# Performance work log

Measured on AMD Instinct MI355X. Metric: run time of the kernel, lower is better.

## Reference

```python
import jax, jax.numpy as jnp
import numpy as np
import math

B, F, N, EMB, H, NC, L = 16, 60, 512, 128, 4, 27, 2
EPS = 1e-5


def _ln(x, g, b):
    m = x.mean(-1, keepdims=True)
    v = ((x - m) ** 2).mean(-1, keepdims=True)
    return (x - m) / jnp.sqrt(v + EPS) * g + b


def _bn(x, g, b):
    # BatchNorm1d in training mode: batch statistics over dim 0
    m = x.mean(0)
    v = ((x - m) ** 2).mean(0)
    return (x - m) / jnp.sqrt(v + EPS) * g + b


def _pos_encoding(S, D):
    pos = jnp.arange(S, dtype=jnp.float32)[:, None]
    div = jnp.exp(jnp.arange(0, D, 2, dtype=jnp.float32) * (-math.log(10000.0) / D))
    ang = pos * div  # [S, D/2]
    return jnp.stack([jnp.sin(ang), jnp.cos(ang)], axis=-1).reshape(S, D)


def setup_inputs():
    key = jax.random.key(0)
    ks = jax.random.split(key, 16)
    rn = lambda i, shape, s: (jax.random.normal(ks[i], shape) * s).astype(jnp.float32)
    z = lambda *shape: jnp.zeros(shape, jnp.float32)
    o = lambda *shape: jnp.ones(shape, jnp.float32)
    return {
        "x": jax.random.normal(ks[0], (B, F, N, 3), dtype=jnp.float32),
        "frame_length": jax.random.randint(ks[1], (B,), 1, F + 1, dtype=jnp.int32),
        # PointNet encoder (shared per-point MLP 3->64->128->EMB, max-pool)
        "enc_w1": rn(2, (3, 64), 0.3), "enc_b1": z(64),
        "enc_w2": rn(3, (64, 128), 0.1), "enc_b2": z(128),
        "enc_w3": rn(4, (128, EMB), 0.1), "enc_b3": z(EMB),
        "cls_token": rn(5, (1, 1, EMB), 0.02), "cls_pos": rn(6, (1, 1, EMB), 0.02),
        # 2-layer post-norm TransformerEncoder (d=128, h=4, ff=256)
        "in_w": rn(7, (L, 3 * EMB, EMB), 0.05), "in_b": z(L, 3 * EMB),
        "out_w": rn(8, (L, EMB, EMB), 0.05), "out_b": z(L, EMB),
        "ln1_g": o(L, EMB), "ln1_b": z(L, EMB),
        "ff1_w": rn(9, (L, 256, EMB), 0.05), "ff1_b": z(L, 256),
        "ff2_w": rn(10, (L, EMB, 256), 0.05), "ff2_b": z(L, EMB),
        "ln2_g": o(L, EMB), "ln2_b": z(L, EMB),
        # MLP head (weights stored [in, out])
        "fc1_w": rn(11, (2 * EMB, 128), 0.05), "fc1_b": z(128),
        "bn1_g": o(128), "bn1_b": z(128),
        "fc15_w": rn(12, (128, 64), 0.05), "fc15_b": z(64),
        "bn15_g": o(64), "bn15_b": z(64),
        "fc2_w": rn(13, (64, 32), 0.05), "fc2_b": z(32),
        "bn2_g": o(32), "bn2_b": z(32),
        "fc_w": rn(14, (32, NC), 0.05), "fc_b": z(NC),
    }


def _forward(x, frame_length, enc_w1, enc_b1, enc_w2, enc_b2, enc_w3, enc_b3,
             cls_token, cls_pos, in_w, in_b, out_w, out_b, ln1_g, ln1_b,
             ff1_w, ff1_b, ff2_w, ff2_b, ln2_g, ln2_b,
             fc1_w, fc1_b, bn1_g, bn1_b, fc15_w, fc15_b, bn15_g, bn15_b,
             fc2_w, fc2_b, bn2_g, bn2_b, fc_w, fc_b):
    dh = EMB // H
    # --- per-frame PointNet encoder, vectorized over (B, F) ---
    # (replaces the ragged Python loop; padded frames are masked to zero below,
    #  exactly matching y = zeros(...) filled only for valid frames)
    h = jax.nn.relu(jnp.einsum('bfnc,cd->bfnd', x, enc_w1) + enc_b1)
    h = jax.nn.relu(h @ enc_w2 + enc_b2)
    h = h @ enc_w3 + enc_b3
    y = h.max(axis=2)  # [B, F, EMB]
    valid = (jnp.arange(F)[None, :] < frame_length[:, None])  # [B, F]
    y = jnp.where(valid[..., None], y, 0.0)

    # --- cls token + sinusoidal positions ---
    pe = _pos_encoding(F, EMB)[None]  # [1, F, EMB]
    y = jnp.concatenate([jnp.broadcast_to(cls_token, (B, 1, EMB)), y], axis=1)
    pos = jnp.concatenate([cls_pos, pe], axis=1)
    y = y + pos  # [B, F+1, EMB]

    S = F + 1
    kpm = jnp.arange(S)[None, :] >= (frame_length + 1)[:, None]  # True = pad
    bias = jnp.where(kpm, -1e9, 0.0)[:, None, None, :]  # [B,1,1,S]

    for l in range(L):
        qkv = y @ in_w[l].T + in_b[l]  # [B,S,3*EMB]
        q, k, v = jnp.split(qkv, 3, axis=-1)
        q = q.reshape(B, S, H, dh).transpose(0, 2, 1, 3)
        k = k.reshape(B, S, H, dh).transpose(0, 2, 1, 3)
        v = v.reshape(B, S, H, dh).transpose(0, 2, 1, 3)
        scores = jnp.einsum('bhqd,bhkd->bhqk', q, k) / math.sqrt(dh) + bias
        attn = jax.nn.softmax(scores, axis=-1)
        o = jnp.einsum('bhqk,bhkd->bhqd', attn, v).transpose(0, 2, 1, 3).reshape(B, S, EMB)
        y = _ln(y + (o @ out_w[l].T + out_b[l]), ln1_g[l], ln1_b[l])
        ff = jax.nn.relu(y @ ff1_w[l].T + ff1_b[l]) @ ff2_w[l].T + ff2_b[l]
        y = _ln(y + ff, ln2_g[l], ln2_b[l])

    # --- ragged gather: cls output + last valid frame output ---
    z1 = y[:, 0, :]
    z2 = y[jnp.arange(B), frame_length]  # position frame_length[i] (cls offset)
    zc = jnp.concatenate([z1, z2], axis=1)  # [B, 2*EMB]

    lrelu = lambda t: jax.nn.leaky_relu(t, negative_slope=0.2)
    y1 = lrelu(_bn(zc @ fc1_w + fc1_b, bn1_g, bn1_b))
    y1 = lrelu(_bn(y1 @ fc15_w + fc15_b, bn15_g, bn15_b))
    y1 = lrelu(_bn(y1 @ fc2_w + fc2_b, bn2_g, bn2_b))
    return y1 @ fc_w + fc_b  # [B, NC]


def reference(x, frame_length, enc_w1, enc_b1, enc_w2, enc_b2, enc_w3, enc_b3,
              cls_token, cls_pos, in_w, in_b, out_w, out_b, ln1_g, ln1_b,
              ff1_w, ff1_b, ff2_w, ff2_b, ln2_g, ln2_b,
              fc1_w, fc1_b, bn1_g, bn1_b, fc15_w, fc15_b, bn15_g, bn15_b,
              fc2_w, fc2_b, bn2_g, bn2_b, fc_w, fc_b):
    return _forward(x, frame_length, enc_w1, enc_b1, enc_w2, enc_b2, enc_w3, enc_b3,
                    cls_token, cls_pos, in_w, in_b, out_w, out_b, ln1_g, ln1_b,
                    ff1_w, ff1_b, ff2_w, ff2_b, ln2_g, ln2_b,
                    fc1_w, fc1_b, bn1_g, bn1_b, fc15_w, fc15_b, bn15_g, bn15_b,
                    fc2_w, fc2_b, bn2_g, bn2_b, fc_w, fc_b)
```

## Files before the change

kernel.cpp:

```cpp
#include <hip/hip_runtime.h>
#include <math.h>

#define SS 61
#define EPSV 1e-5f

typedef __attribute__((ext_vector_type(8))) short bf16x8;
typedef __attribute__((ext_vector_type(4))) short s16x4;
typedef __attribute__((ext_vector_type(4))) float f32x4;

__device__ __forceinline__ short f2bf(float f){
  return __builtin_bit_cast(short, (__bf16)f);
}
__device__ __forceinline__ float bf2f(short s){
  unsigned u = ((unsigned)(unsigned short)s) << 16;
  return __builtin_bit_cast(float, u);
}
__device__ __forceinline__ bf16x8 pack8(f32x4 lo, f32x4 hi){
  bf16x8 r;
  r[0]=f2bf(lo[0]); r[1]=f2bf(lo[1]); r[2]=f2bf(lo[2]); r[3]=f2bf(lo[3]);
  r[4]=f2bf(hi[0]); r[5]=f2bf(hi[1]); r[6]=f2bf(hi[2]); r[7]=f2bf(hi[3]);
  return r;
}
__device__ __forceinline__ s16x4 pack4(f32x4 v){
  s16x4 r; r[0]=f2bf(v[0]); r[1]=f2bf(v[1]); r[2]=f2bf(v[2]); r[3]=f2bf(v[3]); return r;
}
#define YI(t,d) (((t)<<7) + ((d) ^ (((t)&7)<<2)))
#define OI(t,e) (((t)<<7) + ((e) ^ (((t)&7)<<2)))
#define FI(t,e) (((t)<<8) + ((e) ^ (((t)&7)<<2)))
#define VI(k,d) (((k)<<5) + ((d) ^ (((k)&7)<<2)))
#define H1A(pt,idx) ((pt)*128 + (((idx)*2) ^ (((pt)&7)<<4)))
#define H2A(pt,idx) ((pt)*256 + (((idx)*2) ^ (((pt)&15)<<4)))

__global__ __launch_bounds__(256) void prep_kernel(
    const float* __restrict__ ew1, const float* __restrict__ eb1,
    const float* __restrict__ ew2, const float* __restrict__ ew3,
    const float* __restrict__ in_w, const float* __restrict__ ow,
    const float* __restrict__ f1w, const float* __restrict__ f2w,
    const float* __restrict__ fc1w, const float* __restrict__ fc15w,
    const float* __restrict__ fc2w, const float* __restrict__ fcw,
    unsigned short* __restrict__ wbf)
{
  int s = blockIdx.x * 256 + threadIdx.x;
  int i = s & 7, lane = (s >> 3) & 63, frag = s >> 9;
  int c = lane & 15, g = lane >> 4;
  int sig = 16 * (i >> 2) + 4 * g + (i & 3);
  unsigned short outv;
  if (frag < 8) {
    int mt = frag & 3;
    float base = (sig < 3) ? ew1[sig * 64 + 16 * mt + c]
               : (sig == 3 ? eb1[16 * mt + c] : 0.f);
    short hv = f2bf(base);
    if (frag < 4) outv = (unsigned short)hv;
    else { float rv = base - bf2f(hv); outv = (unsigned short)f2bf(rv); }
  } else if (frag < 24) {
    int f = frag - 8; int mt = f >> 1, ks = f & 1;
    outv = (unsigned short)f2bf(ew2[(32 * ks + sig) * 128 + 16 * mt + c]);
  } else if (frag < 56) {
    int f = frag - 24; int mt = f >> 2, ks = f & 3;
    outv = (unsigned short)f2bf(ew3[(32 * ks + sig) * 128 + 16 * mt + c]);
  } else if (frag < 568) {
    int f = frag - 56; int l = f >> 8; f &= 255;
    float v;
    if (f < 96) { int tq = f >> 2, ks = f & 3;
      v = in_w[(size_t)l * 49152 + (size_t)(16 * tq + c) * 128 + 32 * ks + sig]; }
    else if (f < 128) { int f3 = f - 96; int t = f3 >> 2, ks = f3 & 3;
      v = ow[(size_t)l * 16384 + (size_t)(16 * t + c) * 128 + 32 * ks + sig]; }
    else if (f < 192) { int f3 = f - 128; int t = f3 >> 2, ks = f3 & 3;
      v = f1w[(size_t)l * 32768 + (size_t)(16 * t + c) * 128 + 32 * ks + sig]; }
    else { int f3 = f - 192; int t = f3 >> 3, ks = f3 & 7;
      v = f2w[(size_t)l * 32768 + (size_t)(16 * t + c) * 256 + 32 * ks + sig]; }
    outv = (unsigned short)f2bf(v);
  } else {
    int f = frag - 568;
    float v; int hl;
    if (f < 128) { hl = f >> 6; int f6 = f & 63; int mt = f6 >> 3, ks = f6 & 7;
      v = fc1w[(32 * ks + sig) * 128 + 16 * mt + c]; }
    else if (f < 160) { int f2_ = f - 128; hl = f2_ >> 4; int f4 = f2_ & 15; int mt = f4 >> 2, ks = f4 & 3;
      v = fc15w[(32 * ks + sig) * 64 + 16 * mt + c]; }
    else if (f < 168) { int f2_ = f - 160; hl = f2_ >> 2; int f4 = f2_ & 3; int mt = f4 >> 1, ks = f4 & 1;
      v = fc2w[(32 * ks + sig) * 32 + 16 * mt + c]; }
    else { int f2_ = f - 168; hl = f2_ >> 1; int mt = f2_ & 1; int m = 16 * mt + c;
      v = (m < 27) ? fcw[sig * 27 + m] : 0.f; }
    short hv = f2bf(v);
    outv = hl ? (unsigned short)f2bf(v - bf2f(hv)) : (unsigned short)hv;
  }
  wbf[s] = outv;
}

__global__ __launch_bounds__(256) void enc_kernel(
    const float* __restrict__ x,
    const float* __restrict__ eb2, const float* __restrict__ eb3,
    const unsigned short* __restrict__ wbf,
    float* __restrict__ ymax)
{
  __shared__ __align__(16) unsigned short h1p[64 * 64];
  __shared__ __align__(16) unsigned short h2p[64 * 128];
  __shared__ float pmerge[2][128];
  const int tid = threadIdx.x, lane = tid & 63, wv = tid >> 6;
  const int c = lane & 15, g = lane >> 4;
  const int mh = wv & 1, gh = wv >> 1;
  const int frame = blockIdx.x;
  const bf16x8* wf = (const bf16x8*)wbf;

  bf16x8 A1h[4], A1l[4];
#pragma unroll
  for (int mt = 0; mt < 4; mt++) { A1h[mt] = wf[mt * 64 + lane]; A1l[mt] = wf[(4 + mt) * 64 + lane]; }
  bf16x8 A2f[4][2];
#pragma unroll
  for (int j = 0; j < 4; j++)
#pragma unroll
    for (int ks = 0; ks < 2; ks++) A2f[j][ks] = wf[(8 + (4 * mh + j) * 2 + ks) * 64 + lane];
  bf16x8 A3f[4][4];
#pragma unroll
  for (int j = 0; j < 4; j++)
#pragma unroll
    for (int ks = 0; ks < 4; ks++) A3f[j][ks] = wf[(24 + (4 * mh + j) * 4 + ks) * 64 + lane];
  f32x4 b2v[4];
#pragma unroll
  for (int j = 0; j < 4; j++) b2v[j] = *(const f32x4*)(eb2 + 16 * (4 * mh + j) + 4 * g);

  f32x4 pool[4];
#pragma unroll
  for (int j = 0; j < 4; j++) pool[j] = {-1e30f, -1e30f, -1e30f, -1e30f};

  const float* xf = x + (size_t)frame * 1536;
  float nx0, nx1, nx2;
  { const float* xp = xf + (16 * wv + c) * 3; nx0 = xp[0]; nx1 = xp[1]; nx2 = xp[2]; }

  const int ptw = 16 * wv + c;

  for (int t = 0; t < 8; t++) {
    const float x0 = nx0, x1 = nx1, x2 = nx2;
    if (t < 7) {
      const float* xp = xf + ((t + 1) * 64 + 16 * wv + c) * 3;
      nx0 = xp[0]; nx1 = xp[1]; nx2 = xp[2];
    }
    bf16x8 bxh = {0,0,0,0,0,0,0,0}, bxl = {0,0,0,0,0,0,0,0};
    if (g == 0) {
      short h0 = f2bf(x0), h1_ = f2bf(x1), h2_ = f2bf(x2);
      bxh[0] = h0; bxh[1] = h1_; bxh[2] = h2_; bxh[3] = (short)0x3F80;
      bxl[0] = f2bf(x0 - bf2f(h0)); bxl[1] = f2bf(x1 - bf2f(h1_)); bxl[2] = f2bf(x2 - bf2f(h2_));
    }
#pragma unroll
    for (int mt = 0; mt < 4; mt++) {
      f32x4 a = {0.f, 0.f, 0.f, 0.f};
      a = __builtin_amdgcn_mfma_f32_16x16x32_bf16(A1h[mt], bxh, a, 0, 0, 0);
      a = __builtin_amdgcn_mfma_f32_16x16x32_bf16(A1h[mt], bxl, a, 0, 0, 0);
      a = __builtin_amdgcn_mfma_f32_16x16x32_bf16(A1l[mt], bxh, a, 0, 0, 0);
      f32x4 rl;
#pragma unroll
      for (int r = 0; r < 4; r++) rl[r] = fmaxf(a[r], 0.f);
      *(s16x4*)((char*)h1p + H1A(ptw, (mt >> 1) * 32 + g * 8 + (mt & 1) * 4)) = pack4(rl);
    }
    __syncthreads();
    bf16x8 B2[2][2];
#pragma unroll
    for (int gi = 0; gi < 2; gi++)
#pragma unroll
      for (int ks = 0; ks < 2; ks++) {
        const int pt = 16 * (2 * gh + gi) + c;
        B2[gi][ks] = *(const bf16x8*)((const char*)h1p + H1A(pt, ks * 32 + g * 8));
      }
#pragma unroll
    for (int j = 0; j < 4; j++)
#pragma unroll
      for (int gi = 0; gi < 2; gi++) {
        f32x4 a = b2v[j];
        a = __builtin_amdgcn_mfma_f32_16x16x32_bf16(A2f[j][0], B2[gi][0], a, 0, 0, 0);
        a = __builtin_amdgcn_mfma_f32_16x16x32_bf16(A2f[j][1], B2[gi][1], a, 0, 0, 0);
        f32x4 rl;
#pragma unroll
        for (int r = 0; r < 4; r++) rl[r] = fmaxf(a[r], 0.f);
        const int mt = 4 * mh + j;
        const int pt = 16 * (2 * gh + gi) + c;
        *(s16x4*)((char*)h2p + H2A(pt, (mt >> 1) * 32 + g * 8 + (mt & 1) * 4)) = pack4(rl);
      }
    __syncthreads();
    bf16x8 B3[2][4];
#pragma unroll
    for (int gi = 0; gi < 2; gi++)
#pragma unroll
      for (int ks = 0; ks < 4; ks++) {
        const int pt = 16 * (2 * gh + gi) + c;
        B3[gi][ks] = *(const bf16x8*)((const char*)h2p + H2A(pt, ks * 32 + g * 8));
      }
#pragma unroll
    for (int j = 0; j < 4; j++)
#pragma unroll
      for (int gi = 0; gi < 2; gi++) {
        f32x4 a = {0.f, 0.f, 0.f, 0.f};
        a = __builtin_amdgcn_mfma_f32_16x16x32_bf16(A3f[j][0], B3[gi][0], a, 0, 0, 0);
        a = __builtin_amdgcn_mfma_f32_16x16x32_bf16(A3f[j][1], B3[gi][1], a, 0, 0, 0);
        a = __builtin_amdgcn_mfma_f32_16x16x32_bf16(A3f[j][2], B3[gi][2], a, 0, 0, 0);
        a = __builtin_amdgcn_mfma_f32_16x16x32_bf16(A3f[j][3], B3[gi][3], a, 0, 0, 0);
#pragma unroll
        for (int r = 0; r < 4; r++) pool[j][r] = fmaxf(pool[j][r], a[r]);
      }
  }

#pragma unroll
  for (int j = 0; j < 4; j++)
#pragma unroll
    for (int r = 0; r < 4; r++) {
      float v = pool[j][r];
      v = fmaxf(v, __shfl_xor(v, 1, 64));
      v = fmaxf(v, __shfl_xor(v, 2, 64));
      v = fmaxf(v, __shfl_xor(v, 4, 64));
      v = fmaxf(v, __shfl_xor(v, 8, 64));
      pool[j][r] = v;
    }
  if (c == 0) {
#pragma unroll
    for (int j = 0; j < 4; j++)
      *(f32x4*)&pmerge[gh][64 * mh + 16 * j + 4 * g] = pool[j];
  }
  __syncthreads();
  if (tid < 128)
    ymax[(size_t)frame * 128 + tid] = fmaxf(pmerge[0][tid], pmerge[1][tid]) + eb3[tid];
}

__global__ __launch_bounds__(512, 1) void xformer_kernel(
    const float* __restrict__ ymax, const int* __restrict__ fl,
    const float* __restrict__ ctok, const float* __restrict__ cpos,
    const unsigned short* __restrict__ wbf,
    const float* __restrict__ in_b, const float* __restrict__ ob,
    const float* __restrict__ l1g, const float* __restrict__ l1b,
    const float* __restrict__ f1b, const float* __restrict__ f2b,
    const float* __restrict__ l2g, const float* __restrict__ l2b,
    float* __restrict__ zbuf)
{
  __shared__ __align__(16) float ylds[64 * 128];
  __shared__ __align__(16) unsigned short ubuf[64 * 256];
  __shared__ __align__(16) unsigned short kq4[2][8][4][64][4];
  const int b = blockIdx.x, tid = threadIdx.x;
  const int w8 = tid >> 6, lane = tid & 63, c = lane & 15, g = lane >> 4;
  const int h = w8 >> 1, sub = w8 & 1;
  const int flb = fl[b];
  const float scl = 0.17677669529663687f;

  for (int it = 0; it < 16; it++) {
    int idx = it * 512 + tid;
    int t = idx >> 7, d = idx & 127;
    float v;
    if (t == 0) v = ctok[d] + cpos[d];
    else if (t <= 60) {
      int f = t - 1;
      float ym = (f < flb) ? ymax[(size_t)(b * 60 + f) * 128 + d] : 0.f;
      float dv = __expf((float)(d & ~1) * (-0.07195578416f));
      float ang = (float)f * dv;
      v = ym + ((d & 1) ? __cosf(ang) : __sinf(ang));
    } else v = 0.f;
    ylds[YI(t, d)] = v;
  }
  __syncthreads();

  for (int l = 0; l < 2; l++) {
    const unsigned short* WL = wbf + 28672 + (size_t)l * 131072;
    const bf16x8* wq  = (const bf16x8*)WL;
    const bf16x8* wo  = (const bf16x8*)(WL + 49152);
    const bf16x8* w1p = (const bf16x8*)(WL + 65536);
    const bf16x8* w2p = (const bf16x8*)(WL + 98304);
    unsigned short* vb = ubuf + 8192 + h * 2048;

    {
      bf16x8 yB[4][4];
#pragma unroll
      for (int nt = 0; nt < 4; nt++)
#pragma unroll
        for (int ks = 0; ks < 4; ks++) {
          f32x4 lo = *(const f32x4*)&ylds[YI(16 * nt + c, 32 * ks + 4 * g)];
          f32x4 hi = *(const f32x4*)&ylds[YI(16 * nt + c, 32 * ks + 16 + 4 * g)];
          yB[nt][ks] = pack8(lo, hi);
        }
#pragma unroll
      for (int p = 0; p < 3; p++) {
        const int tq = p * 8 + w8;
        bf16x8 Af[4];
#pragma unroll
        for (int ks = 0; ks < 4; ks++) Af[ks] = wq[(tq * 4 + ks) * 64 + lane];
        f32x4 bias = *(const f32x4*)(in_b + l * 384 + p * 128 + 16 * w8 + 4 * g);
        f32x4 acc[4];
#pragma unroll
        for (int nt = 0; nt < 4; nt++) acc[nt] = bias;
#pragma unroll
        for (int ks = 0; ks < 4; ks++)
#pragma unroll
          for (int nt = 0; nt < 4; nt++)
            acc[nt] = __builtin_amdgcn_mfma_f32_16x16x32_bf16(Af[ks], yB[nt][ks], acc[nt], 0, 0, 0);
        if (p == 2) {
#pragma unroll
          for (int nt = 0; nt < 4; nt++)
            *(s16x4*)&vb[VI(16 * nt + c, 16 * sub + 4 * g)] = pack4(acc[nt]);
        } else {
#pragma unroll
          for (int nt = 0; nt < 4; nt++) {
            f32x4 sv = acc[nt];
            if (p == 0) sv = sv * scl;
            *(s16x4*)&kq4[p][w8][nt][lane][0] = pack4(sv);
          }
        }
      }
    }
    __syncthreads();

    {
      bf16x8 Ak[4], Bq2[2];
#pragma unroll
      for (int kt = 0; kt < 4; kt++) {
        s16x4 lo = *(const s16x4*)&kq4[1][2 * h][kt][lane][0];
        s16x4 hi = *(const s16x4*)&kq4[1][2 * h + 1][kt][lane][0];
        Ak[kt] = __builtin_shufflevector(lo, hi, 0, 1, 2, 3, 4, 5, 6, 7);
      }
#pragma unroll
      for (int j = 0; j < 2; j++) {
        s16x4 lo = *(const s16x4*)&kq4[0][2 * h][2 * sub + j][lane][0];
        s16x4 hi = *(const s16x4*)&kq4[0][2 * h + 1][2 * sub + j][lane][0];
        Bq2[j] = __builtin_shufflevector(lo, hi, 0, 1, 2, 3, 4, 5, 6, 7);
      }
      f32x4 St[4][2];
#pragma unroll
      for (int kt = 0; kt < 4; kt++)
#pragma unroll
        for (int j = 0; j < 2; j++) {
          f32x4 z = {0.f, 0.f, 0.f, 0.f};
          St[kt][j] = __builtin_amdgcn_mfma_f32_16x16x32_bf16(Ak[kt], Bq2[j], z, 0, 0, 0);
        }
#pragma unroll
      for (int j = 0; j < 2; j++) {
        float m = -1e30f;
#pragma unroll
        for (int kt = 0; kt < 4; kt++)
#pragma unroll
          for (int r = 0; r < 4; r++) {
            const int kp = 16 * kt + 4 * g + r;
            float s = St[kt][j][r];
            s = (kp > flb) ? -1e30f : s;
            St[kt][j][r] = s;
            m = fmaxf(m, s);
          }
        m = fmaxf(m, __shfl_xor(m, 16, 64));
        m = fmaxf(m, __shfl_xor(m, 32, 64));
        float sum = 0.f;
#pragma unroll
        for (int kt = 0; kt < 4; kt++)
#pragma unroll
          for (int r = 0; r < 4; r++) {
            float p = __expf(St[kt][j][r] - m);
            St[kt][j][r] = p;
            sum += p;
          }
        sum += __shfl_xor(sum, 16, 64);
        sum += __shfl_xor(sum, 32, 64);
        const float inv = 1.f / sum;
#pragma unroll
        for (int kt = 0; kt < 4; kt++)
#pragma unroll
          for (int r = 0; r < 4; r++) St[kt][j][r] *= inv;
      }
      bf16x8 Bp[2][2];
#pragma unroll
      for (int j = 0; j < 2; j++)
#pragma unroll
        for (int ks = 0; ks < 2; ks++) {
          bf16x8 r;
#pragma unroll
          for (int i = 0; i < 8; i++) r[i] = f2bf(St[2 * ks + (i >> 2)][j][i & 3]);
          Bp[j][ks] = r;
        }
      bf16x8 Av[2][2];
#pragma unroll
      for (int dt = 0; dt < 2; dt++)
#pragma unroll
        for (int ks = 0; ks < 2; ks++) {
          bf16x8 r;
#pragma unroll
          for (int i = 0; i < 8; i++) {
            const int kp = 32 * ks + 16 * (i >> 2) + 4 * g + (i & 3);
            r[i] = (short)vb[VI(kp, 16 * dt + c)];
          }
          Av[dt][ks] = r;
        }
#pragma unroll
      for (int dt = 0; dt < 2; dt++)
#pragma unroll
        for (int j = 0; j < 2; j++) {
          f32x4 z = {0.f, 0.f, 0.f, 0.f};
          z = __builtin_amdgcn_mfma_f32_16x16x32_bf16(Av[dt][0], Bp[j][0], z, 0, 0, 0);
          z = __builtin_amdgcn_mfma_f32_16x16x32_bf16(Av[dt][1], Bp[j][1], z, 0, 0, 0);
          *(s16x4*)&ubuf[OI(16 * (2 * sub + j) + c, 32 * h + 16 * dt + 4 * g)] = pack4(z);
        }
    }
    __syncthreads();

    {
      bf16x8 Bo[4][4];
#pragma unroll
      for (int nt = 0; nt < 4; nt++)
#pragma unroll
        for (int ks = 0; ks < 4; ks++) {
          s16x4 lo = *(const s16x4*)&ubuf[OI(16 * nt + c, 32 * ks + 4 * g)];
          s16x4 hi = *(const s16x4*)&ubuf[OI(16 * nt + c, 32 * ks + 16 + 4 * g)];
          Bo[nt][ks] = __builtin_shufflevector(lo, hi, 0, 1, 2, 3, 4, 5, 6, 7);
        }
      const int j0 = 16 * w8;
      bf16x8 Af[4];
#pragma unroll
      for (int ks = 0; ks < 4; ks++) Af[ks] = wo[(w8 * 4 + ks) * 64 + lane];
      f32x4 bias = *(const f32x4*)(ob + l * 128 + j0 + 4 * g);
      f32x4 acc[4];
#pragma unroll
      for (int nt = 0; nt < 4; nt++) acc[nt] = bias;
#pragma unroll
      for (int ks = 0; ks < 4; ks++)
#pragma unroll
        for (int nt = 0; nt < 4; nt++)
          acc[nt] = __builtin_amdgcn_mfma_f32_16x16x32_bf16(Af[ks], Bo[nt][ks], acc[nt], 0, 0, 0);
#pragma unroll
      for (int nt = 0; nt < 4; nt++) {
        float* yp = &ylds[YI(16 * nt + c, j0 + 4 * g)];
        *(f32x4*)yp = *(const f32x4*)yp + acc[nt];
      }
    }
    __syncthreads();
    {
      const int t = 8 * w8 + (lane >> 3);
      const int s = lane & 7;
      f32x4 vv[4];
      float s1 = 0.f, s2 = 0.f;
#pragma unroll
      for (int k = 0; k < 4; k++) {
        vv[k] = *(const f32x4*)&ylds[YI(t, s * 16 + 4 * k)];
#pragma unroll
        for (int r = 0; r < 4; r++) { s1 += vv[k][r]; s2 = fmaf(vv[k][r], vv[k][r], s2); }
      }
      s1 += __shfl_xor(s1, 1, 64); s1 += __shfl_xor(s1, 2, 64); s1 += __shfl_xor(s1, 4, 64);
      s2 += __shfl_xor(s2, 1, 64); s2 += __shfl_xor(s2, 2, 64); s2 += __shfl_xor(s2, 4, 64);
      const float mean = s1 * 0.0078125f;
      const float var  = s2 * 0.0078125f - mean * mean;
      const float inv  = rsqrtf(var + EPSV);
#pragma unroll
      for (int k = 0; k < 4; k++) {
        f32x4 gg = *(const f32x4*)(l1g + l * 128 + s * 16 + 4 * k);
        f32x4 bb = *(const f32x4*)(l1b + l * 128 + s * 16 + 4 * k);
        f32x4 o;
#pragma unroll
        for (int r = 0; r < 4; r++) o[r] = (vv[k][r] - mean) * inv * gg[r] + bb[r];
        *(f32x4*)&ylds[YI(t, s * 16 + 4 * k)] = o;
      }
    }
    __syncthreads();

    {
      bf16x8 yB[4][4];
#pragma unroll
      for (int nt = 0; nt < 4; nt++)
#pragma unroll
        for (int ks = 0; ks < 4; ks++) {
          f32x4 lo = *(const f32x4*)&ylds[YI(16 * nt + c, 32 * ks + 4 * g)];
          f32x4 hi = *(const f32x4*)&ylds[YI(16 * nt + c, 32 * ks + 16 + 4 * g)];
          yB[nt][ks] = pack8(lo, hi);
        }
#pragma unroll
      for (int half = 0; half < 2; half++) {
        const int t16 = 8 * half + w8;
        bf16x8 Af[4];
#pragma unroll
        for (int ks = 0; ks < 4; ks++) Af[ks] = w1p[(t16 * 4 + ks) * 64 + lane];
        f32x4 bias = *(const f32x4*)(f1b + l * 256 + 16 * t16 + 4 * g);
        f32x4 acc[4];
#pragma unroll
        for (int nt = 0; nt < 4; nt++) acc[nt] = bias;
#pragma unroll
        for (int ks = 0; ks < 4; ks++)
#pragma unroll
          for (int nt = 0; nt < 4; nt++)
            acc[nt] = __builtin_amdgcn_mfma_f32_16x16x32_bf16(Af[ks], yB[nt][ks], acc[nt], 0, 0, 0);
#pragma unroll
        for (int nt = 0; nt < 4; nt++) {
          f32x4 rl;
#pragma unroll
          for (int r = 0; r < 4; r++) rl[r] = fmaxf(acc[nt][r], 0.f);
          *(s16x4*)&ubuf[FI(16 * nt + c, 16 * t16 + 4 * g)] = pack4(rl);
        }
      }
    }
    __syncthreads();
    {
      f32x4 acc[4];
      f32x4 bias = *(const f32x4*)(f2b + l * 128 + 16 * w8 + 4 * g);
#pragma unroll
      for (int nt = 0; nt < 4; nt++) acc[nt] = bias;
#pragma unroll
      for (int ks = 0; ks < 8; ks++) {
        bf16x8 Af = w2p[(w8 * 8 + ks) * 64 + lane];
        bf16x8 Bf[4];
#pragma unroll
        for (int nt = 0; nt < 4; nt++) {
          s16x4 lo = *(const s16x4*)&ubuf[FI(16 * nt + c, 32 * ks + 4 * g)];
          s16x4 hi = *(const s16x4*)&ubuf[FI(16 * nt + c, 32 * ks + 16 + 4 * g)];
          Bf[nt] = __builtin_shufflevector(lo, hi, 0, 1, 2, 3, 4, 5, 6, 7);
        }
#pragma unroll
        for (int nt = 0; nt < 4; nt++)
          acc[nt] = __builtin_amdgcn_mfma_f32_16x16x32_bf16(Af, Bf[nt], acc[nt], 0, 0, 0);
      }
#pragma unroll
      for (int nt = 0; nt < 4; nt++) {
        float* yp = &ylds[YI(16 * nt + c, 16 * w8 + 4 * g)];
        *(f32x4*)yp = *(const f32x4*)yp + acc[nt];
      }
    }
    __syncthreads();
    {
      const int t = 8 * w8 + (lane >> 3);
      const int s = lane & 7;
      f32x4 vv[4];
      float s1 = 0.f, s2 = 0.f;
#pragma unroll
      for (int k = 0; k < 4; k++) {
        vv[k] = *(const f32x4*)&ylds[YI(t, s * 16 + 4 * k)];
#pragma unroll
        for (int r = 0; r < 4; r++) { s1 += vv[k][r]; s2 = fmaf(vv[k][r], vv[k][r], s2); }
      }
      s1 += __shfl_xor(s1, 1, 64); s1 += __shfl_xor(s1, 2, 64); s1 += __shfl_xor(s1, 4, 64);
      s2 += __shfl_xor(s2, 1, 64); s2 += __shfl_xor(s2, 2, 64); s2 += __shfl_xor(s2, 4, 64);
      const float mean = s1 * 0.0078125f;
      const float var  = s2 * 0.0078125f - mean * mean;
      const float inv  = rsqrtf(var + EPSV);
#pragma unroll
      for (int k = 0; k < 4; k++) {
        f32x4 gg = *(const f32x4*)(l2g + l * 128 + s * 16 + 4 * k);
        f32x4 bb = *(const f32x4*)(l2b + l * 128 + s * 16 + 4 * k);
        f32x4 o;
#pragma unroll
        for (int r = 0; r < 4; r++) o[r] = (vv[k][r] - mean) * inv * gg[r] + bb[r];
        *(f32x4*)&ylds[YI(t, s * 16 + 4 * k)] = o;
      }
    }
    __syncthreads();
  }

  if (tid < 256) {
    const int d = tid;
    float v = (d < 128) ? ylds[YI(0, d)] : ylds[YI(flb, d - 128)];
    zbuf[d * 16 + b] = v;
  }
}

__device__ __forceinline__ void buildB(const float* src, int ks, int g, int c,
                                       bf16x8& bh, bf16x8& bl){
#pragma unroll
  for (int i = 0; i < 8; i++) {
    int k = 32 * ks + 16 * (i >> 2) + 4 * g + (i & 3);
    float v = src[k * 16 + c];
    short hv = f2bf(v);
    bh[i] = hv; bl[i] = f2bf(v - bf2f(hv));
  }
}
__device__ __forceinline__ void bn_lrelu_store(f32x4 acc, int ch0, int c,
    const float* __restrict__ gg, const float* __restrict__ bb, float* dst){
#pragma unroll
  for (int r = 0; r < 4; r++) {
    float v = acc[r];
    float s1 = v, s2 = v * v;
    s1 += __shfl_xor(s1, 1, 64); s2 += __shfl_xor(s2, 1, 64);
    s1 += __shfl_xor(s1, 2, 64); s2 += __shfl_xor(s2, 2, 64);
    s1 += __shfl_xor(s1, 4, 64); s2 += __shfl_xor(s2, 4, 64);
    s1 += __shfl_xor(s1, 8, 64); s2 += __shfl_xor(s2, 8, 64);
    const float m = s1 * (1.f / 16.f);
    const float var = s2 * (1.f / 16.f) - m * m;
    const float scl = gg[ch0 + r] / sqrtf(var + EPSV);
    const float sh = bb[ch0 + r] - m * scl;
    float o = v * scl + sh;
    o = (o > 0.f) ? o : 0.2f * o;
    dst[(ch0 + r) * 16 + c] = o;
  }
}

__global__ __launch_bounds__(256, 1) void head_kernel(
    const float* __restrict__ zt, const unsigned short* __restrict__ wbf,
    const float* __restrict__ fc1b, const float* __restrict__ bn1g, const float* __restrict__ bn1b,
    const float* __restrict__ fc15b, const float* __restrict__ bn15g, const float* __restrict__ bn15b,
    const float* __restrict__ fc2b, const float* __restrict__ bn2g, const float* __restrict__ bn2b,
    const float* __restrict__ fcb, float* __restrict__ out)
{
  __shared__ float zs[256 * 16];
  __shared__ float t1s[128 * 16];
  __shared__ float t15s[64 * 16];
  __shared__ float t2s[32 * 16];
  const int tid = threadIdx.x, lane = tid & 63, wv = tid >> 6;
  const int c = lane & 15, g = lane >> 4;
  const bf16x8* wf = (const bf16x8*)wbf;

  for (int idx = tid; idx < 4096; idx += 256) zs[idx] = zt[idx];
  __syncthreads();

  {
    f32x4 acc[2];
#pragma unroll
    for (int j = 0; j < 2; j++) {
      const int ch0 = 16 * (2 * wv + j) + 4 * g;
      f32x4 a;
#pragma unroll
      for (int r = 0; r < 4; r++) a[r] = fc1b[ch0 + r];
      acc[j] = a;
    }
#pragma unroll
    for (int ks = 0; ks < 8; ks++) {
      bf16x8 bh, bl; buildB(zs, ks, g, c, bh, bl);
#pragma unroll
      for (int j = 0; j < 2; j++) {
        const int mt = 2 * wv + j;
        bf16x8 Ah = wf[(568 + mt * 8 + ks) * 64 + lane];
        bf16x8 Al = wf[(632 + mt * 8 + ks) * 64 + lane];
        acc[j] = __builtin_amdgcn_mfma_f32_16x16x32_bf16(Ah, bh, acc[j], 0, 0, 0);
        acc[j] = __builtin_amdgcn_mfma_f32_16x16x32_bf16(Ah, bl, acc[j], 0, 0, 0);
        acc[j] = __builtin_amdgcn_mfma_f32_16x16x32_bf16(Al, bh, acc[j], 0, 0, 0);
      }
    }
#pragma unroll
    for (int j = 0; j < 2; j++)
      bn_lrelu_store(acc[j], 16 * (2 * wv + j) + 4 * g, c, bn1g, bn1b, t1s);
  }
  __syncthreads();

  {
    const int ch0 = 16 * wv + 4 * g;
    f32x4 a;
#pragma unroll
    for (int r = 0; r < 4; r++) a[r] = fc15b[ch0 + r];
#pragma unroll
    for (int ks = 0; ks < 4; ks++) {
      bf16x8 bh, bl; buildB(t1s, ks, g, c, bh, bl);
      bf16x8 Ah = wf[(696 + wv * 4 + ks) * 64 + lane];
      bf16x8 Al = wf[(712 + wv * 4 + ks) * 64 + lane];
      a = __builtin_amdgcn_mfma_f32_16x16x32_bf16(Ah, bh, a, 0, 0, 0);
      a = __builtin_amdgcn_mfma_f32_16x16x32_bf16(Ah, bl, a, 0, 0, 0);
      a = __builtin_amdgcn_mfma_f32_16x16x32_bf16(Al, bh, a, 0, 0, 0);
    }
    bn_lrelu_store(a, ch0, c, bn15g, bn15b, t15s);
  }
  __syncthreads();

  if (wv < 2) {
    const int ch0 = 16 * wv + 4 * g;
    f32x4 a;
#pragma unroll
    for (int r = 0; r < 4; r++) a[r] = fc2b[ch0 + r];
#pragma unroll
    for (int ks = 0; ks < 2; ks++) {
      bf16x8 bh, bl; buildB(t15s, ks, g, c, bh, bl);
      bf16x8 Ah = wf[(728 + wv * 2 + ks) * 64 + lane];
      bf16x8 Al = wf[(732 + wv * 2 + ks) * 64 + lane];
      a = __builtin_amdgcn_mfma_f32_16x16x32_bf16(Ah, bh, a, 0, 0, 0);
      a = __builtin_amdgcn_mfma_f32_16x16x32_bf16(Ah, bl, a, 0, 0, 0);
      a = __builtin_amdgcn_mfma_f32_16x16x32_bf16(Al, bh, a, 0, 0, 0);
    }
    bn_lrelu_store(a, ch0, c, bn2g, bn2b, t2s);
  }
  __syncthreads();

  if (wv < 2) {
    f32x4 a;
#pragma unroll
    for (int r = 0; r < 4; r++) {
      const int ch = 16 * wv + 4 * g + r;
      a[r] = (ch < 27) ? fcb[ch] : 0.f;
    }
    bf16x8 bh, bl; buildB(t2s, 0, g, c, bh, bl);
    bf16x8 Ah = wf[(736 + wv) * 64 + lane];
    bf16x8 Al = wf[(738 + wv) * 64 + lane];
    a = __builtin_amdgcn_mfma_f32_16x16x32_bf16(Ah, bh, a, 0, 0, 0);
    a = __builtin_amdgcn_mfma_f32_16x16x32_bf16(Ah, bl, a, 0, 0, 0);
    a = __builtin_amdgcn_mfma_f32_16x16x32_bf16(Al, bh, a, 0, 0, 0);
#pragma unroll
    for (int r = 0; r < 4; r++) {
      const int ch = 16 * wv + 4 * g + r;
      if (ch < 27) out[c * 27 + ch] = a[r];
    }
  }
}

extern "C" void kernel_launch(void* const* d_in, const int* in_sizes, int n_in,
                              void* d_out, int out_size, void* d_ws, size_t ws_size,
                              hipStream_t stream)
{
  const float* x    = (const float*)d_in[0];
  const int*   fl   = (const int*)d_in[1];
  const float* ew1  = (const float*)d_in[2];  const float* eb1 = (const float*)d_in[3];
  const float* ew2  = (const float*)d_in[4];  const float* eb2 = (const float*)d_in[5];
  const float* ew3  = (const float*)d_in[6];  const float* eb3 = (const float*)d_in[7];
  const float* ctok = (const float*)d_in[8];  const float* cpos = (const float*)d_in[9];
  const float* in_w = (const float*)d_in[10]; const float* in_b = (const float*)d_in[11];
  const float* ow   = (const float*)d_in[12]; const float* ob   = (const float*)d_in[13];
  const float* l1g  = (const float*)d_in[14]; const float* l1b  = (const float*)d_in[15];
  const float* f1w  = (const float*)d_in[16]; const float* f1b  = (const float*)d_in[17];
  const float* f2w  = (const float*)d_in[18]; const float* f2b  = (const float*)d_in[19];
  const float* l2g  = (const float*)d_in[20]; const float* l2b  = (const float*)d_in[21];
  const float* fc1w = (const float*)d_in[22]; const float* fc1b = (const float*)d_in[23];
  const float* bn1g = (const float*)d_in[24]; const float* bn1b = (const float*)d_in[25];
  const float* fc15w= (const float*)d_in[26]; const float* fc15b= (const float*)d_in[27];
  const float* bn15g= (const float*)d_in[28]; const float* bn15b= (const float*)d_in[29];
  const float* fc2w = (const float*)d_in[30]; const float* fc2b = (const float*)d_in[31];
  const float* bn2g = (const float*)d_in[32]; const float* bn2b = (const float*)d_in[33];
  const float* fcw  = (const float*)d_in[34]; const float* fcb  = (const float*)d_in[35];
  float* out = (float*)d_out;

  char* w = (char*)d_ws;
  float* ymax = (float*)w;
  float* zbuf = (float*)(w + 491520);
  unsigned short* wbf = (unsigned short*)(w + 507904);

  prep_kernel<<<1480, 256, 0, stream>>>(ew1, eb1, ew2, ew3, in_w, ow, f1w, f2w,
                                        fc1w, fc15w, fc2w, fcw, wbf);
  enc_kernel<<<960, 256, 0, stream>>>(x, eb2, eb3, wbf, ymax);
  xformer_kernel<<<16, 512, 0, stream>>>(ymax, fl, ctok, cpos, wbf, in_b, ob,
                                         l1g, l1b, f1b, f2b, l2g, l2b, zbuf);
  head_kernel<<<1, 256, 0, stream>>>(zbuf, wbf, fc1b, bn1g, bn1b,
                                     fc15b, bn15g, bn15b, fc2b, bn2g, bn2b, fcb, out);
}
```

Before: 80.37 us.

## Keep encoder layer-1 activations in registers and double-buffer layer-2 LDS exchange

Each wave now computes the first PointNet layer for its own point groups and feeds the MFMA outputs straight into the layer-2 B operand in registers, dropping the h1 LDS round trip and one barrier per iteration. Layer-2 outputs are split: the half each wave produced is reused from registers, and only the other half is read from a double-buffered LDS array indexed by iteration parity. This removes a syncthreads and part of the LDS traffic per tile. The cost is that layer 1 is computed redundantly by both waves sharing a point group, plus extra register pressure and a swizzle/shuffle fixup for the lane permutation.

```diff
diff --git a/kernel.cpp b/kernel.cpp
--- a/kernel.cpp
+++ b/kernel.cpp
@@ -28,8 +28,6 @@
 #define OI(t,e) (((t)<<7) + ((e) ^ (((t)&7)<<2)))
 #define FI(t,e) (((t)<<8) + ((e) ^ (((t)&7)<<2)))
 #define VI(k,d) (((k)<<5) + ((d) ^ (((k)&7)<<2)))
-#define H1A(pt,idx) ((pt)*128 + (((idx)*2) ^ (((pt)&7)<<4)))
-#define H2A(pt,idx) ((pt)*256 + (((idx)*2) ^ (((pt)&15)<<4)))
 
 __global__ __launch_bounds__(256) void prep_kernel(
     const float* __restrict__ ew1, const float* __restrict__ eb1,
@@ -93,8 +91,7 @@
     const unsigned short* __restrict__ wbf,
     float* __restrict__ ymax)
 {
-  __shared__ __align__(16) unsigned short h1p[64 * 64];
-  __shared__ __align__(16) unsigned short h2p[64 * 128];
+  __shared__ __align__(16) unsigned short h2p[2][2][64][64];
   __shared__ float pmerge[2][128];
   const int tid = threadIdx.x, lane = tid & 63, wv = tid >> 6;
   const int c = lane & 15, g = lane >> 4;
@@ -124,43 +121,59 @@
   for (int j = 0; j < 4; j++) pool[j] = {-1e30f, -1e30f, -1e30f, -1e30f};
 
   const float* xf = x + (size_t)frame * 1536;
-  float nx0, nx1, nx2;
-  { const float* xp = xf + (16 * wv + c) * 3; nx0 = xp[0]; nx1 = xp[1]; nx2 = xp[2]; }
-
-  const int ptw = 16 * wv + c;
+  float nx[2][3];
+#pragma unroll
+  for (int gi = 0; gi < 2; gi++) {
+    const float* xp = xf + (16 * (2 * gh + gi) + c) * 3;
+    nx[gi][0] = xp[0]; nx[gi][1] = xp[1]; nx[gi][2] = xp[2];
+  }
+  const int swap8 = c >> 3;
 
   for (int t = 0; t < 8; t++) {
-    const float x0 = nx0, x1 = nx1, x2 = nx2;
+    float cx[2][3];
+#pragma unroll
+    for (int gi = 0; gi < 2; gi++) {
+      cx[gi][0] = nx[gi][0]; cx[gi][1] = nx[gi][1]; cx[gi][2] = nx[gi][2];
+    }
     if (t < 7) {
-      const float* xp = xf + ((t + 1) * 64 + 16 * wv + c) * 3;
-      nx0 = xp[0]; nx1 = xp[1]; nx2 = xp[2];
-    }
-    bf16x8 bxh = {0,0,0,0,0,0,0,0}, bxl = {0,0,0,0,0,0,0,0};
-    if (g == 0) {
-      short h0 = f2bf(x0), h1_ = f2bf(x1), h2_ = f2bf(x2);
-      bxh[0] = h0; bxh[1] = h1_; bxh[2] = h2_; bxh[3] = (short)0x3F80;
-      bxl[0] = f2bf(x0 - bf2f(h0)); bxl[1] = f2bf(x1 - bf2f(h1_)); bxl[2] = f2bf(x2 - bf2f(h2_));
-    }
-#pragma unroll
-    for (int mt = 0; mt < 4; mt++) {
-      f32x4 a = {0.f, 0.f, 0.f, 0.f};
-      a = __builtin_amdgcn_mfma_f32_16x16x32_bf16(A1h[mt], bxh, a, 0, 0, 0);
-      a = __builtin_amdgcn_mfma_f32_16x16x32_bf16(A1h[mt], bxl, a, 0, 0, 0);
-      a = __builtin_amdgcn_mfma_f32_16x16x32_bf16(A1l[mt], bxh, a, 0, 0, 0);
-      f32x4 rl;
-#pragma unroll
-      for (int r = 0; r < 4; r++) rl[r] = fmaxf(a[r], 0.f);
-      *(s16x4*)((char*)h1p + H1A(ptw, (mt >> 1) * 32 + g * 8 + (mt & 1) * 4)) = pack4(rl);
-    }
-    __syncthreads();
+#pragma unroll
+      for (int gi = 0; gi < 2; gi++) {
+        const float* xp = xf + ((t + 1) * 64 + 16 * (2 * gh + gi) + c) * 3;
+        nx[gi][0] = xp[0]; nx[gi][1] = xp[1]; nx[gi][2] = xp[2];
+      }
+    }
+    f32x4 d1[2][4];
+#pragma unroll
+    for (int gi = 0; gi < 2; gi++) {
+      bf16x8 bxh = {0,0,0,0,0,0,0,0}, bxl = {0,0,0,0,0,0,0,0};
+      if (g == 0) {
+        short h0 = f2bf(cx[gi][0]), h1_ = f2bf(cx[gi][1]), h2_ = f2bf(cx[gi][2]);
+        bxh[0] = h0; bxh[1] = h1_; bxh[2] = h2_; bxh[3] = (short)0x3F80;
+        bxl[0] = f2bf(cx[gi][0] - bf2f(h0));
+        bxl[1] = f2bf(cx[gi][1] - bf2f(h1_));
+        bxl[2] = f2bf(cx[gi][2] - bf2f(h2_));
+      }
+#pragma unroll
+      for (int mt = 0; mt < 4; mt++) {
+        f32x4 a = {0.f, 0.f, 0.f, 0.f};
+        a = __builtin_amdgcn_mfma_f32_16x16x32_bf16(A1h[mt], bxh, a, 0, 0, 0);
+        a = __builtin_amdgcn_mfma_f32_16x16x32_bf16(A1h[mt], bxl, a, 0, 0, 0);
+        a = __builtin_amdgcn_mfma_f32_16x16x32_bf16(A1l[mt], bxh, a, 0, 0, 0);
+        d1[gi][mt] = a;
+      }
+    }
     bf16x8 B2[2][2];
 #pragma unroll
     for (int gi = 0; gi < 2; gi++)
 #pragma unroll
       for (int ks = 0; ks < 2; ks++) {
-        const int pt = 16 * (2 * gh + gi) + c;
-        B2[gi][ks] = *(const bf16x8*)((const char*)h1p + H1A(pt, ks * 32 + g * 8));
-      }
+        bf16x8 r;
+#pragma unroll
+        for (int i = 0; i < 8; i++)
+          r[i] = f2bf(fmaxf(d1[gi][2 * ks + (i >> 2)][i & 3], 0.f));
+        B2[gi][ks] = r;
+      }
+    f32x4 acc2[4][2];
 #pragma unroll
     for (int j = 0; j < 4; j++)
 #pragma unroll
@@ -168,31 +181,52 @@
         f32x4 a = b2v[j];
         a = __builtin_amdgcn_mfma_f32_16x16x32_bf16(A2f[j][0], B2[gi][0], a, 0, 0, 0);
         a = __builtin_amdgcn_mfma_f32_16x16x32_bf16(A2f[j][1], B2[gi][1], a, 0, 0, 0);
+        acc2[j][gi] = a;
+      }
+    s16x4 q[4][2];
+    unsigned short* hb = &h2p[t & 1][mh][0][0];
+#pragma unroll
+    for (int j = 0; j < 4; j++)
+#pragma unroll
+      for (int gi = 0; gi < 2; gi++) {
         f32x4 rl;
 #pragma unroll
-        for (int r = 0; r < 4; r++) rl[r] = fmaxf(a[r], 0.f);
-        const int mt = 4 * mh + j;
+        for (int r = 0; r < 4; r++) rl[r] = fmaxf(acc2[j][gi][r], 0.f);
+        q[j][gi] = pack4(rl);
         const int pt = 16 * (2 * gh + gi) + c;
-        *(s16x4*)((char*)h2p + H2A(pt, (mt >> 1) * 32 + g * 8 + (mt & 1) * 4)) = pack4(rl);
-      }
+        const int idxh2 = ((j >> 1) * 32 + g * 8 + (j & 1) * 4) * 2;
+        const int off = (idxh2 ^ ((pt & 7) << 4)) ^ (swap8 << 3);
+        *(s16x4*)((char*)hb + pt * 128 + off) = q[j][gi];
+      }
+    bf16x8 B3o[2][2];
+#pragma unroll
+    for (int gi = 0; gi < 2; gi++)
+#pragma unroll
+      for (int ksl = 0; ksl < 2; ksl++)
+        B3o[gi][ksl] = __builtin_shufflevector(q[2 * ksl][gi], q[2 * ksl + 1][gi],
+                                               0, 1, 2, 3, 4, 5, 6, 7);
     __syncthreads();
-    bf16x8 B3[2][4];
+    const unsigned short* ho = &h2p[t & 1][1 - mh][0][0];
+    bf16x8 Bx[2][2];
 #pragma unroll
     for (int gi = 0; gi < 2; gi++)
 #pragma unroll
-      for (int ks = 0; ks < 4; ks++) {
+      for (int ksl = 0; ksl < 2; ksl++) {
         const int pt = 16 * (2 * gh + gi) + c;
-        B3[gi][ks] = *(const bf16x8*)((const char*)h2p + H2A(pt, ks * 32 + g * 8));
+        const int off = (64 * ksl + 16 * g) ^ ((pt & 7) << 4);
+        bf16x8 v = *(const bf16x8*)((const char*)ho + pt * 128 + off);
+        bf16x8 vs = __builtin_shufflevector(v, v, 4, 5, 6, 7, 0, 1, 2, 3);
+        Bx[gi][ksl] = swap8 ? vs : v;
       }
 #pragma unroll
     for (int j = 0; j < 4; j++)
 #pragma unroll
       for (int gi = 0; gi < 2; gi++) {
         f32x4 a = {0.f, 0.f, 0.f, 0.f};
-        a = __builtin_amdgcn_mfma_f32_16x16x32_bf16(A3f[j][0], B3[gi][0], a, 0, 0, 0);
-        a = __builtin_amdgcn_mfma_f32_16x16x32_bf16(A3f[j][1], B3[gi][1], a, 0, 0, 0);
-        a = __builtin_amdgcn_mfma_f32_16x16x32_bf16(A3f[j][2], B3[gi][2], a, 0, 0, 0);
-        a = __builtin_amdgcn_mfma_f32_16x16x32_bf16(A3f[j][3], B3[gi][3], a, 0, 0, 0);
+        a = __builtin_amdgcn_mfma_f32_16x16x32_bf16(A3f[j][2 * mh + 0], B3o[gi][0], a, 0, 0, 0);
+        a = __builtin_amdgcn_mfma_f32_16x16x32_bf16(A3f[j][2 * mh + 1], B3o[gi][1], a, 0, 0, 0);
+        a = __builtin_amdgcn_mfma_f32_16x16x32_bf16(A3f[j][2 * (1 - mh) + 0], Bx[gi][0], a, 0, 0, 0);
+        a = __builtin_amdgcn_mfma_f32_16x16x32_bf16(A3f[j][2 * (1 - mh) + 1], Bx[gi][1], a, 0, 0, 0);
 #pragma unroll
         for (int r = 0; r < 4; r++) pool[j][r] = fmaxf(pool[j][r], a[r]);
       }
```

Result: slower. 131.0 us (+63.0%).

## Encode one frame per wavefront with register-resident MLP chaining

Applied to the files above, without the earlier changes.

The PointNet encoder now gives each wavefront a whole frame instead of splitting a frame across four waves through shared memory. Layer outputs are repacked in registers straight into the next MFMA B operand, which removes the LDS staging buffers and the block-wide barriers between layers. Each wave now keeps all 8 output tiles of weights in registers, and the grid shrinks from 960 to 240 blocks. The cost is much higher register pressure, forced by launch_bounds(256,1), and far fewer waves to hide latency on a chip with 256 CUs.

```diff
diff --git a/kernel.cpp b/kernel.cpp
--- a/kernel.cpp
+++ b/kernel.cpp
@@ -28,8 +28,6 @@
 #define OI(t,e) (((t)<<7) + ((e) ^ (((t)&7)<<2)))
 #define FI(t,e) (((t)<<8) + ((e) ^ (((t)&7)<<2)))
 #define VI(k,d) (((k)<<5) + ((d) ^ (((k)&7)<<2)))
-#define H1A(pt,idx) ((pt)*128 + (((idx)*2) ^ (((pt)&7)<<4)))
-#define H2A(pt,idx) ((pt)*256 + (((idx)*2) ^ (((pt)&15)<<4)))
 
 __global__ __launch_bounds__(256) void prep_kernel(
     const float* __restrict__ ew1, const float* __restrict__ eb1,
@@ -87,136 +85,137 @@
   wbf[s] = outv;
 }
 
-__global__ __launch_bounds__(256) void enc_kernel(
+__global__ __launch_bounds__(256, 1) void enc_kernel(
     const float* __restrict__ x,
     const float* __restrict__ eb2, const float* __restrict__ eb3,
     const unsigned short* __restrict__ wbf,
     float* __restrict__ ymax)
 {
-  __shared__ __align__(16) unsigned short h1p[64 * 64];
-  __shared__ __align__(16) unsigned short h2p[64 * 128];
-  __shared__ float pmerge[2][128];
   const int tid = threadIdx.x, lane = tid & 63, wv = tid >> 6;
   const int c = lane & 15, g = lane >> 4;
-  const int mh = wv & 1, gh = wv >> 1;
-  const int frame = blockIdx.x;
+  const int frame = blockIdx.x * 4 + wv;
   const bf16x8* wf = (const bf16x8*)wbf;
 
   bf16x8 A1h[4], A1l[4];
 #pragma unroll
   for (int mt = 0; mt < 4; mt++) { A1h[mt] = wf[mt * 64 + lane]; A1l[mt] = wf[(4 + mt) * 64 + lane]; }
-  bf16x8 A2f[4][2];
-#pragma unroll
-  for (int j = 0; j < 4; j++)
-#pragma unroll
-    for (int ks = 0; ks < 2; ks++) A2f[j][ks] = wf[(8 + (4 * mh + j) * 2 + ks) * 64 + lane];
-  bf16x8 A3f[4][4];
-#pragma unroll
-  for (int j = 0; j < 4; j++)
-#pragma unroll
-    for (int ks = 0; ks < 4; ks++) A3f[j][ks] = wf[(24 + (4 * mh + j) * 4 + ks) * 64 + lane];
-  f32x4 b2v[4];
-#pragma unroll
-  for (int j = 0; j < 4; j++) b2v[j] = *(const f32x4*)(eb2 + 16 * (4 * mh + j) + 4 * g);
-
-  f32x4 pool[4];
-#pragma unroll
-  for (int j = 0; j < 4; j++) pool[j] = {-1e30f, -1e30f, -1e30f, -1e30f};
+  bf16x8 A2f[8][2];
+#pragma unroll
+  for (int mt = 0; mt < 8; mt++)
+#pragma unroll
+    for (int ks = 0; ks < 2; ks++) A2f[mt][ks] = wf[(8 + mt * 2 + ks) * 64 + lane];
+  bf16x8 A3f[8][4];
+#pragma unroll
+  for (int mt = 0; mt < 8; mt++)
+#pragma unroll
+    for (int ks = 0; ks < 4; ks++) A3f[mt][ks] = wf[(24 + mt * 4 + ks) * 64 + lane];
+  f32x4 b2v[8];
+#pragma unroll
+  for (int mt = 0; mt < 8; mt++) b2v[mt] = *(const f32x4*)(eb2 + 16 * mt + 4 * g);
+
+  f32x4 pool[8];
+#pragma unroll
+  for (int mt = 0; mt < 8; mt++) pool[mt] = {-1e30f, -1e30f, -1e30f, -1e30f};
 
   const float* xf = x + (size_t)frame * 1536;
-  float nx0, nx1, nx2;
-  { const float* xp = xf + (16 * wv + c) * 3; nx0 = xp[0]; nx1 = xp[1]; nx2 = xp[2]; }
-
-  const int ptw = 16 * wv + c;
-
-  for (int t = 0; t < 8; t++) {
-    const float x0 = nx0, x1 = nx1, x2 = nx2;
-    if (t < 7) {
-      const float* xp = xf + ((t + 1) * 64 + 16 * wv + c) * 3;
-      nx0 = xp[0]; nx1 = xp[1]; nx2 = xp[2];
-    }
-    bf16x8 bxh = {0,0,0,0,0,0,0,0}, bxl = {0,0,0,0,0,0,0,0};
-    if (g == 0) {
-      short h0 = f2bf(x0), h1_ = f2bf(x1), h2_ = f2bf(x2);
-      bxh[0] = h0; bxh[1] = h1_; bxh[2] = h2_; bxh[3] = (short)0x3F80;
-      bxl[0] = f2bf(x0 - bf2f(h0)); bxl[1] = f2bf(x1 - bf2f(h1_)); bxl[2] = f2bf(x2 - bf2f(h2_));
-    }
-#pragma unroll
-    for (int mt = 0; mt < 4; mt++) {
-      f32x4 a = {0.f, 0.f, 0.f, 0.f};
-      a = __builtin_amdgcn_mfma_f32_16x16x32_bf16(A1h[mt], bxh, a, 0, 0, 0);
-      a = __builtin_amdgcn_mfma_f32_16x16x32_bf16(A1h[mt], bxl, a, 0, 0, 0);
-      a = __builtin_amdgcn_mfma_f32_16x16x32_bf16(A1l[mt], bxh, a, 0, 0, 0);
-      f32x4 rl;
-#pragma unroll
-      for (int r = 0; r < 4; r++) rl[r] = fmaxf(a[r], 0.f);
-      *(s16x4*)((char*)h1p + H1A(ptw, (mt >> 1) * 32 + g * 8 + (mt & 1) * 4)) = pack4(rl);
-    }
-    __syncthreads();
-    bf16x8 B2[2][2];
-#pragma unroll
-    for (int gi = 0; gi < 2; gi++)
+  float nx[2][3];
+#pragma unroll
+  for (int nt = 0; nt < 2; nt++) {
+    const float* xp = xf + (16 * nt + c) * 3;
+    nx[nt][0] = xp[0]; nx[nt][1] = xp[1]; nx[nt][2] = xp[2];
+  }
+
+  for (int t = 0; t < 16; t++) {
+    float cx[2][3];
+#pragma unroll
+    for (int nt = 0; nt < 2; nt++) {
+      cx[nt][0] = nx[nt][0]; cx[nt][1] = nx[nt][1]; cx[nt][2] = nx[nt][2];
+    }
+    if (t < 15) {
+#pragma unroll
+      for (int nt = 0; nt < 2; nt++) {
+        const float* xp = xf + ((t + 1) * 32 + 16 * nt + c) * 3;
+        nx[nt][0] = xp[0]; nx[nt][1] = xp[1]; nx[nt][2] = xp[2];
+      }
+    }
+#pragma unroll
+    for (int nt = 0; nt < 2; nt++) {
+      bf16x8 bxh = {0,0,0,0,0,0,0,0}, bxl = {0,0,0,0,0,0,0,0};
+      if (g == 0) {
+        short h0 = f2bf(cx[nt][0]), h1_ = f2bf(cx[nt][1]), h2_ = f2bf(cx[nt][2]);
+        bxh[0] = h0; bxh[1] = h1_; bxh[2] = h2_; bxh[3] = (short)0x3F80;
+        bxl[0] = f2bf(cx[nt][0] - bf2f(h0));
+        bxl[1] = f2bf(cx[nt][1] - bf2f(h1_));
+        bxl[2] = f2bf(cx[nt][2] - bf2f(h2_));
+      }
+      f32x4 d1[4];
+#pragma unroll
+      for (int mt = 0; mt < 4; mt++) {
+        f32x4 a = {0.f, 0.f, 0.f, 0.f};
+        a = __builtin_amdgcn_mfma_f32_16x16x32_bf16(A1h[mt], bxh, a, 0, 0, 0);
+        a = __builtin_amdgcn_mfma_f32_16x16x32_bf16(A1h[mt], bxl, a, 0, 0, 0);
+        a = __builtin_amdgcn_mfma_f32_16x16x32_bf16(A1l[mt], bxh, a, 0, 0, 0);
+        d1[mt] = a;
+      }
+      bf16x8 B2[2];
 #pragma unroll
       for (int ks = 0; ks < 2; ks++) {
-        const int pt = 16 * (2 * gh + gi) + c;
-        B2[gi][ks] = *(const bf16x8*)((const char*)h1p + H1A(pt, ks * 32 + g * 8));
-      }
-#pragma unroll
-    for (int j = 0; j < 4; j++)
-#pragma unroll
-      for (int gi = 0; gi < 2; gi++) {
-        f32x4 a = b2v[j];
-        a = __builtin_amdgcn_mfma_f32_16x16x32_bf16(A2f[j][0], B2[gi][0], a, 0, 0, 0);
-        a = __builtin_amdgcn_mfma_f32_16x16x32_bf16(A2f[j][1], B2[gi][1], a, 0, 0, 0);
-        f32x4 rl;
-#pragma unroll
-        for (int r = 0; r < 4; r++) rl[r] = fmaxf(a[r], 0.f);
-        const int mt = 4 * mh + j;
-        const int pt = 16 * (2 * gh + gi) + c;
-        *(s16x4*)((char*)h2p + H2A(pt, (mt >> 1) * 32 + g * 8 + (mt & 1) * 4)) = pack4(rl);
-      }
-    __syncthreads();
-    bf16x8 B3[2][4];
-#pragma unroll
-    for (int gi = 0; gi < 2; gi++)
+        bf16x8 r;
+#pragma unroll
+        for (int i = 0; i < 8; i++)
+          r[i] = f2bf(fmaxf(d1[2 * ks + (i >> 2)][i & 3], 0.f));
+        B2[ks] = r;
+      }
+      f32x4 acc2[8];
+#pragma unroll
+      for (int mt = 0; mt < 8; mt++) {
+        f32x4 a = b2v[mt];
+        a = __builtin_amdgcn_mfma_f32_16x16x32_bf16(A2f[mt][0], B2[0], a, 0, 0, 0);
+        a = __builtin_amdgcn_mfma_f32_16x16x32_bf16(A2f[mt][1], B2[1], a, 0, 0, 0);
+        acc2[mt] = a;
+      }
+      bf16x8 B3[4];
 #pragma unroll
       for (int ks = 0; ks < 4; ks++) {
-        const int pt = 16 * (2 * gh + gi) + c;
-        B3[gi][ks] = *(const bf16x8*)((const char*)h2p + H2A(pt, ks * 32 + g * 8));
-      }
-#pragma unroll
-    for (int j = 0; j < 4; j++)
-#pragma unroll
-      for (int gi = 0; gi < 2; gi++) {
+        bf16x8 r;
+#pragma unroll
+        for (int i = 0; i < 8; i++)
+          r[i] = f2bf(fmaxf(acc2[2 * ks + (i >> 2)][i & 3], 0.f));
+        B3[ks] = r;
+      }
+#pragma unroll
+      for (int mt = 0; mt < 8; mt++) {
         f32x4 a = {0.f, 0.f, 0.f, 0.f};
-        a = __builtin_amdgcn_mfma_f32_16x16x32_bf16(A3f[j][0], B3[gi][0], a, 0, 0, 0);
-        a = __builtin_amdgcn_mfma_f32_16x16x32_bf16(A3f[j][1], B3[gi][1], a, 0, 0, 0);
-        a = __builtin_amdgcn_mfma_f32_16x16x32_bf16(A3f[j][2], B3[gi][2], a, 0, 0, 0);
-        a = __builtin_amdgcn_mfma_f32_16x16x32_bf16(A3f[j][3], B3[gi][3], a, 0, 0, 0);
-#pragma unroll
-        for (int r = 0; r < 4; r++) pool[j][r] = fmaxf(pool[j][r], a[r]);
-      }
-  }
-
-#pragma unroll
-  for (int j = 0; j < 4; j++)
+        a = __builtin_amdgcn_mfma_f32_16x16x32_bf16(A3f[mt][0], B3[0], a, 0, 0, 0);
+        a = __builtin_amdgcn_mfma_f32_16x16x32_bf16(A3f[mt][1], B3[1], a, 0, 0, 0);
+        a = __builtin_amdgcn_mfma_f32_16x16x32_bf16(A3f[mt][2], B3[2], a, 0, 0, 0);
+        a = __builtin_amdgcn_mfma_f32_16x16x32_bf16(A3f[mt][3], B3[3], a, 0, 0, 0);
+#pragma unroll
+        for (int r = 0; r < 4; r++) pool[mt][r] = fmaxf(pool[mt][r], a[r]);
+      }
+    }
+  }
+
+#pragma unroll
+  for (int mt = 0; mt < 8; mt++)
 #pragma unroll
     for (int r = 0; r < 4; r++) {
-      float v = pool[j][r];
+      float v = pool[mt][r];
       v = fmaxf(v, __shfl_xor(v, 1, 64));
       v = fmaxf(v, __shfl_xor(v, 2, 64));
       v = fmaxf(v, __shfl_xor(v, 4, 64));
       v = fmaxf(v, __shfl_xor(v, 8, 64));
-      pool[j][r] = v;
+      pool[mt][r] = v;
     }
   if (c == 0) {
 #pragma unroll
-    for (int j = 0; j < 4; j++)
-      *(f32x4*)&pmerge[gh][64 * mh + 16 * j + 4 * g] = pool[j];
-  }
-  __syncthreads();
-  if (tid < 128)
-    ymax[(size_t)frame * 128 + tid] = fmaxf(pmerge[0][tid], pmerge[1][tid]) + eb3[tid];
+    for (int mt = 0; mt < 8; mt++)
+#pragma unroll
+      for (int r = 0; r < 4; r++) {
+        const int ch = 16 * mt + 4 * g + r;
+        ymax[(size_t)frame * 128 + ch] = pool[mt][r] + eb3[ch];
+      }
+  }
 }
 
 __global__ __launch_bounds__(512, 1) void xformer_kernel(
@@ -713,7 +712,7 @@
 
   prep_kernel<<<1480, 256, 0, stream>>>(ew1, eb1, ew2, ew3, in_w, ow, f1w, f2w,
                                         fc1w, fc15w, fc2w, fcw, wbf);
-  enc_kernel<<<960, 256, 0, stream>>>(x, eb2, eb3, wbf, ymax);
+  enc_kernel<<<240, 256, 0, stream>>>(x, eb2, eb3, wbf, ymax);
   xformer_kernel<<<16, 512, 0, stream>>>(ymax, fl, ctok, cpos, wbf, in_b, ob,
                                          l1g, l1b, f1b, f2b, l2g, l2b, zbuf);
   head_kernel<<<1, 256, 0, stream>>>(zbuf, wbf, fc1b, bn1g, bn1b,
```

Measured after the change: 81.79 us. About the same (+1.8%).
